# Kernel tuning notes

Hardware: AMD Instinct MI355X
Metric: run time of the kernel (lower is better)

The kernel has to match this reference:

```python
import jax, jax.numpy as jnp
import numpy as np

BOND = 64
RANK = 16
PATCH = 4
SIDE = 64          # num_patches_side = 256 // 4
OUT_C = 3
NODES = [1, 4, 16, 64, 256, 1024]   # per-layer node counts, depth=6
TOTAL_NODES = sum(NODES)            # 1365


def _norm_factor(key, shape):
    f = jax.random.normal(key, shape, dtype=jnp.float32)
    return f / (jnp.linalg.norm(f, axis=-1, keepdims=True) + 1e-8)


def setup_inputs() -> dict:
    key = jax.random.key(0)
    ks = jax.random.split(key, 10)
    B = 128
    x = jax.random.normal(ks[0], (B, 1, BOND), dtype=jnp.float32)
    # All layers' factors concatenated along the node axis (sliced per-layer).
    factor_in = _norm_factor(ks[1], (TOTAL_NODES, RANK, BOND))
    factor_tl = _norm_factor(ks[2], (TOTAL_NODES, RANK, BOND))
    factor_tr = _norm_factor(ks[3], (TOTAL_NODES, RANK, BOND))
    factor_bl = _norm_factor(ks[4], (TOTAL_NODES, RANK, BOND))
    factor_br = _norm_factor(ks[5], (TOTAL_NODES, RANK, BOND))
    scale = 1.0 + 0.02 * jax.random.normal(ks[6], (TOTAL_NODES, RANK), dtype=jnp.float32)
    head_w = jax.random.normal(ks[7], (OUT_C * PATCH * PATCH, BOND), dtype=jnp.float32) * (1.0 / np.sqrt(BOND))
    head_b = jnp.zeros((OUT_C * PATCH * PATCH,), dtype=jnp.float32)
    return {"x": x, "factor_in": factor_in, "factor_tl": factor_tl,
            "factor_tr": factor_tr, "factor_bl": factor_bl, "factor_br": factor_br,
            "scale": scale, "head_w": head_w, "head_b": head_b}


def _forward(x, factor_in, factor_tl, factor_tr, factor_bl, factor_br, scale, head_w, head_b):
    grid = 1
    off = 0
    for n in NODES:  # static loop over depth=6 layers
        fi = factor_in[off:off + n]
        sc = scale[off:off + n]
        lat = jnp.einsum('bni,nri->bnr', x, fi) * sc[None]        # [B,n,r]
        outs = jnp.stack(
            [jnp.einsum('bnr,nro->bno', lat, factor_tl[off:off + n]),
             jnp.einsum('bnr,nro->bno', lat, factor_tr[off:off + n]),
             jnp.einsum('bnr,nro->bno', lat, factor_bl[off:off + n]),
             jnp.einsum('bnr,nro->bno', lat, factor_br[off:off + n])],
            axis=2)                                               # [B,n,4,o]
        x4 = outs + x[:, :, None, :]
        # 'b (h w) (h2 w2) c -> b (h h2 w w2) c' with h=w=grid, h2=w2=2
        b, _, _, c = x4.shape
        x = x4.reshape(b, grid, grid, 2, 2, c).transpose(0, 1, 3, 2, 4, 5).reshape(b, 4 * n, c)
        grid *= 2
        off += n
    # head: Linear(bond -> c*p*p) then 'b (h w) (p1 p2 c) -> b c (h p1) (w p2)'
    y = x @ head_w.T + head_b                                     # [B, 4096, 48]
    b = y.shape[0]
    y = y.reshape(b, SIDE, SIDE, PATCH, PATCH, OUT_C)
    y = y.transpose(0, 5, 1, 3, 2, 4).reshape(b, OUT_C, SIDE * PATCH, SIDE * PATCH)
    return y


def reference(x, factor_in, factor_tl, factor_tr, factor_bl, factor_br, scale, head_w, head_b):
    return _forward(x, factor_in, factor_tl, factor_tr, factor_bl, factor_br, scale, head_w, head_b)
```

## Files before the change

kernel.cpp:

```cpp
#include <hip/hip_runtime.h>

constexpr int BOND = 64;
constexpr int RANK = 16;
constexpr int BT   = 8;
constexpr int NTHR = 256;
constexpr int LPAD = 68;

typedef short  short8 __attribute__((ext_vector_type(8)));
typedef float  f32x4  __attribute__((ext_vector_type(4)));


__device__ __forceinline__ unsigned short f2bf(float f) {
    union { float f; unsigned u; } v; v.f = f;
    unsigned r = v.u + 0x7FFFu + ((v.u >> 16) & 1u);
    return (unsigned short)(r >> 16);
}

__device__ __forceinline__ void node_lat(const float* __restrict__ f_in,
                                         const float* __restrict__ scale,
                                         int fo,
                                         const float* xin,
                                         float* lat,
                                         int tid)
{
    const int b = tid >> 5;
    const int r = (tid >> 1) & 15;
    const int h = tid & 1;
    const float4* fir = (const float4*)(f_in + (size_t)fo * (RANK * BOND) + r * BOND + h * 32);
    const float4* xb  = (const float4*)(xin + b * BOND + h * 32);
    float p = 0.f;
#pragma unroll
    for (int i = 0; i < 8; ++i) {
        const float4 a = fir[i], c = xb[i];
        p += a.x * c.x + a.y * c.y + a.z * c.z + a.w * c.w;
    }
    p += __shfl_xor(p, 1);
    if (h == 0) lat[b * RANK + r] = p * scale[fo * RANK + r];
}

__device__ __forceinline__ void node_children(const float* __restrict__ fd,
                                              const float* xin,
                                              const float* lat,
                                              float* xout,
                                              int bstride,
                                              int tid)
{
    const int o  = tid & 63;
    const int b0 = tid >> 6;
    float f[RANK];
#pragma unroll
    for (int r = 0; r < RANK; ++r) f[r] = fd[r * BOND + o];
#pragma unroll
    for (int bi = 0; bi < BT; bi += 4) {
        const int b = b0 + bi;
        float acc = xin[b * BOND + o];
#pragma unroll
        for (int r = 0; r < RANK; ++r) acc += lat[b * RANK + r] * f[r];
        xout[b * bstride + o] = acc;
    }
}

__global__ __launch_bounds__(NTHR, 3)
void qtree_kernel(const float* __restrict__ x,
                  const float* __restrict__ f_in,
                  const float* __restrict__ f_tl,
                  const float* __restrict__ f_tr,
                  const float* __restrict__ f_bl,
                  const float* __restrict__ f_br,
                  const float* __restrict__ scale,
                  const float* __restrict__ head_w,
                  const float* __restrict__ head_b,
                  float* __restrict__ out)
{
    __shared__ float s_x4[2][BT][BOND];
    __shared__ float s_x5[4][BT][BOND];
    __shared__ float s_leafy[64 * LPAD];
    __shared__ float s_lat[4][BT][RANK];

    const int tid  = threadIdx.x;
    const int lane = tid & 63;
    const int wv   = tid >> 6;
    const int m    = lane & 15;
    const int q    = lane >> 4;
    const int n3   = blockIdx.x;
    const int bg   = blockIdx.y;
    const int jy   = blockIdx.z;
    const int y3   = n3 >> 3, x3 = n3 & 7;

    const float* fdir[4] = { f_tl, f_tr, f_bl, f_br };

    short8 afrag[3][2];
#pragma unroll
    for (int mt = 0; mt < 3; ++mt)
#pragma unroll
        for (int kc = 0; kc < 2; ++kc) {
            const float* src = head_w + (mt * 16 + m) * 64 + kc * 32 + q * 8;
            short8 a;
#pragma unroll
            for (int j = 0; j < 8; ++j) a[j] = (short)f2bf(src[j]);
            afrag[mt][kc] = a;
        }
    f32x4 accinit[3];
#pragma unroll
    for (int mt = 0; mt < 3; ++mt)
#pragma unroll
        for (int r = 0; r < 4; ++r) accinit[mt][r] = head_b[mt * 16 + q * 4 + r];
    const int leaf = wv * 16 + m;
    const int lb = leaf >> 3, ldx = (leaf >> 2) & 1, lc = leaf & 3;
    const int lcy = lc >> 1, lcx = lc & 1;
    const int sy_base = lb * 384 + lcy * 64 + ldx * 8 + lcx * 4;
    int sy_ofs[3][4];
#pragma unroll
    for (int mt = 0; mt < 3; ++mt)
#pragma unroll
        for (int r = 0; r < 4; ++r) {
            const int o = mt * 16 + q * 4 + r;
            sy_ofs[mt][r] = sy_base + (o % 3) * 128 + (o / 12) * 16 + ((o / 3) & 3);
        }

    for (int i4 = tid; i4 < BT * BOND / 4; i4 += NTHR)
        ((float4*)&s_x5[0][0][0])[i4] = ((const float4*)(x + (size_t)bg * BT * BOND))[i4];
    __syncthreads();

    {
        node_lat(f_in, scale, 0, &s_x5[0][0][0], &s_lat[0][0][0], tid);
        __syncthreads();
        const int d = ((y3 >> 2) << 1) | (x3 >> 2);
        node_children(fdir[d], &s_x5[0][0][0], &s_lat[0][0][0], &s_x5[1][0][0], BOND, tid);
        __syncthreads();
    }
    {
        const int fo = 1 + ((y3 >> 2) * 2 + (x3 >> 2));
        node_lat(f_in, scale, fo, &s_x5[1][0][0], &s_lat[0][0][0], tid);
        __syncthreads();
        const int d = (((y3 >> 1) & 1) << 1) | ((x3 >> 1) & 1);
        node_children(fdir[d] + (size_t)fo * RANK * BOND, &s_x5[1][0][0], &s_lat[0][0][0], &s_x5[2][0][0], BOND, tid);
        __syncthreads();
    }
    {
        const int fo = 5 + ((y3 >> 1) * 4 + (x3 >> 1));
        node_lat(f_in, scale, fo, &s_x5[2][0][0], &s_lat[0][0][0], tid);
        __syncthreads();
        const int d = ((y3 & 1) << 1) | (x3 & 1);
        node_children(fdir[d] + (size_t)fo * RANK * BOND, &s_x5[2][0][0], &s_lat[0][0][0], &s_x5[3][0][0], BOND, tid);
        __syncthreads();
    }
    {
        const int fo = 21 + n3;
        node_lat(f_in, scale, fo, &s_x5[3][0][0], &s_lat[0][0][0], tid);
        __syncthreads();
#pragma unroll
        for (int jx = 0; jx < 2; ++jx)
            node_children(fdir[2 * jy + jx] + (size_t)fo * RANK * BOND,
                          &s_x5[3][0][0], &s_lat[0][0][0], &s_x4[jx][0][0], BOND, tid);
        __syncthreads();
    }

    for (int jx = 0; jx < 2; ++jx) {
        const int y4 = 2 * y3 + jy, x4c = 2 * x3 + jx;
        const int fo4 = 85 + y4 * 16 + x4c;
        node_lat(f_in, scale, fo4, &s_x4[jx][0][0], &s_lat[0][0][0], tid);
        __syncthreads();
#pragma unroll
        for (int e = 0; e < 4; ++e)
            node_children(fdir[e] + (size_t)fo4 * RANK * BOND,
                          &s_x4[jx][0][0], &s_lat[0][0][0], &s_x5[e][0][0], BOND, tid);
        __syncthreads();

        int fo5[4];
#pragma unroll
        for (int e = 0; e < 4; ++e) {
            const int dy = e >> 1, dx = e & 1;
            fo5[e] = 341 + (2 * y4 + dy) * 32 + (2 * x4c + dx);
            node_lat(f_in, scale, fo5[e], &s_x5[e][0][0], &s_lat[e][0][0], tid);
        }
        __syncthreads();

        for (int p = 0; p < 2; ++p) {
#pragma unroll
            for (int dx2 = 0; dx2 < 2; ++dx2) {
                const int e = 2 * p + dx2;
#pragma unroll
                for (int c = 0; c < 4; ++c)
                    node_children(fdir[c] + (size_t)fo5[e] * RANK * BOND,
                                  &s_x5[e][0][0], &s_lat[e][0][0],
                                  s_leafy + (dx2 * 4 + c) * LPAD, 8 * LPAD, tid);
            }
            __syncthreads();

            short8 bfrag[2];
#pragma unroll
            for (int kc = 0; kc < 2; ++kc) {
                const float* src = &s_leafy[leaf * LPAD + kc * 32 + q * 8];
                const float4 lo = *(const float4*)src;
                const float4 hi = *(const float4*)(src + 4);
                short8 bq;
                bq[0] = (short)f2bf(lo.x); bq[1] = (short)f2bf(lo.y);
                bq[2] = (short)f2bf(lo.z); bq[3] = (short)f2bf(lo.w);
                bq[4] = (short)f2bf(hi.x); bq[5] = (short)f2bf(hi.y);
                bq[6] = (short)f2bf(hi.z); bq[7] = (short)f2bf(hi.w);
                bfrag[kc] = bq;
            }
            f32x4 acc[3];
#pragma unroll
            for (int mt = 0; mt < 3; ++mt) acc[mt] = accinit[mt];
#pragma unroll
            for (int kc = 0; kc < 2; ++kc)
#pragma unroll
                for (int mt = 0; mt < 3; ++mt)
                    acc[mt] = __builtin_amdgcn_mfma_f32_16x16x32_bf16(afrag[mt][kc], bfrag[kc], acc[mt], 0, 0, 0);
            __syncthreads();

            float* s_y = s_leafy;
#pragma unroll
            for (int mt = 0; mt < 3; ++mt)
#pragma unroll
                for (int r = 0; r < 4; ++r) s_y[sy_ofs[mt][r]] = acc[mt][r];
            __syncthreads();

            const int base_row = (4 * y3 + 2 * jy + p) * 8;
            const int base_col = (4 * x3 + 2 * jx) * 8;
#pragma unroll
            for (int s = 0; s < 3; ++s) {
                const int idx = tid + NTHR * s;
                const int c4  = idx & 3;
                const int r2  = (idx >> 2) & 7;
                const int bc  = idx >> 5;
                const float4 v = *(const float4*)&s_y[(bc * 8 + r2) * 16 + c4 * 4];
                const size_t off = ((size_t)(bg * BT + bc / 3) * 3 + (bc % 3)) * 65536
                                 + (size_t)(base_row + r2) * 256 + base_col + c4 * 4;
                *(float4*)&out[off] = v;
            }
            __syncthreads();
        }
    }
}

extern "C" void kernel_launch(void* const* d_in, const int* in_sizes, int n_in,
                              void* d_out, int out_size, void* d_ws, size_t ws_size,
                              hipStream_t stream) {
    const float* x    = (const float*)d_in[0];
    const float* f_in = (const float*)d_in[1];
    const float* f_tl = (const float*)d_in[2];
    const float* f_tr = (const float*)d_in[3];
    const float* f_bl = (const float*)d_in[4];
    const float* f_br = (const float*)d_in[5];
    const float* sc   = (const float*)d_in[6];
    const float* hw   = (const float*)d_in[7];
    const float* hb   = (const float*)d_in[8];
    float* out = (float*)d_out;

    dim3 grid(64, 16, 2);
    qtree_kernel<<<grid, NTHR, 0, stream>>>(x, f_in, f_tl, f_tr, f_bl, f_br, sc, hw, hb, out);
}
```

Before: 319.6 us.

## Give each wavefront its own two batch rows and drop block-wide barriers

Restructures the tree traversal so each of the four wavefronts owns two batch elements, with private shared-memory buffers for activations, latents, leaf tiles and output staging. All __syncthreads calls go away, since only intra-wave ordering is needed. Leaf activations are stored directly as bf16 in shared memory, so the MFMA B fragment is one vector load instead of a load plus conversion. In exchange, each wave reloads the factor rows for every node (four times the global/L2 factor traffic per block), and the code relies on implicit wave-level ordering of LDS accesses.

```diff
diff --git a/kernel.cpp b/kernel.cpp
--- a/kernel.cpp
+++ b/kernel.cpp
@@ -1,10 +1,6 @@
 #include <hip/hip_runtime.h>
 
-constexpr int BOND = 64;
-constexpr int RANK = 16;
-constexpr int BT   = 8;
 constexpr int NTHR = 256;
-constexpr int LPAD = 68;
 
 typedef short  short8 __attribute__((ext_vector_type(8)));
 typedef float  f32x4  __attribute__((ext_vector_type(4)));
@@ -16,18 +12,18 @@
     return (unsigned short)(r >> 16);
 }
 
-__device__ __forceinline__ void node_lat(const float* __restrict__ f_in,
-                                         const float* __restrict__ scale,
-                                         int fo,
-                                         const float* xin,
-                                         float* lat,
-                                         int tid)
-{
-    const int b = tid >> 5;
-    const int r = (tid >> 1) & 15;
-    const int h = tid & 1;
-    const float4* fir = (const float4*)(f_in + (size_t)fo * (RANK * BOND) + r * BOND + h * 32);
-    const float4* xb  = (const float4*)(xin + b * BOND + h * 32);
+__device__ __forceinline__ void wlat(const float* __restrict__ f_in,
+                                     const float* __restrict__ scale,
+                                     int fo,
+                                     const float (*xin)[64],
+                                     float (*lat)[16],
+                                     int lane)
+{
+    const int b = lane >> 5;
+    const int r = (lane >> 1) & 15;
+    const int h = lane & 1;
+    const float4* fir = (const float4*)(f_in + (size_t)fo * 1024 + r * 64 + h * 32);
+    const float4* xb  = (const float4*)(&xin[b][0] + h * 32);
     float p = 0.f;
 #pragma unroll
     for (int i = 0; i < 8; ++i) {
@@ -35,28 +31,45 @@
         p += a.x * c.x + a.y * c.y + a.z * c.z + a.w * c.w;
     }
     p += __shfl_xor(p, 1);
-    if (h == 0) lat[b * RANK + r] = p * scale[fo * RANK + r];
-}
-
-__device__ __forceinline__ void node_children(const float* __restrict__ fd,
-                                              const float* xin,
-                                              const float* lat,
-                                              float* xout,
-                                              int bstride,
-                                              int tid)
-{
-    const int o  = tid & 63;
-    const int b0 = tid >> 6;
-    float f[RANK];
-#pragma unroll
-    for (int r = 0; r < RANK; ++r) f[r] = fd[r * BOND + o];
-#pragma unroll
-    for (int bi = 0; bi < BT; bi += 4) {
-        const int b = b0 + bi;
-        float acc = xin[b * BOND + o];
-#pragma unroll
-        for (int r = 0; r < RANK; ++r) acc += lat[b * RANK + r] * f[r];
-        xout[b * bstride + o] = acc;
+    if (h == 0) lat[b][r] = p * scale[fo * 16 + r];
+}
+
+__device__ __forceinline__ void wchild(const float* __restrict__ fd,
+                                       const float (*xin)[64],
+                                       const float (*lat)[16],
+                                       float (*xout)[64],
+                                       int lane)
+{
+    const int o = lane;
+    float f[16];
+#pragma unroll
+    for (int r = 0; r < 16; ++r) f[r] = fd[r * 64 + o];
+#pragma unroll
+    for (int b = 0; b < 2; ++b) {
+        float acc = xin[b][o];
+#pragma unroll
+        for (int r = 0; r < 16; ++r) acc += lat[b][r] * f[r];
+        xout[b][o] = acc;
+    }
+}
+
+__device__ __forceinline__ void wchild_leaf(const float* __restrict__ fd,
+                                            const float (*xin)[64],
+                                            const float (*lat)[16],
+                                            unsigned short* leaf,
+                                            int nbase,
+                                            int lane)
+{
+    const int o = lane;
+    float f[16];
+#pragma unroll
+    for (int r = 0; r < 16; ++r) f[r] = fd[r * 64 + o];
+#pragma unroll
+    for (int b = 0; b < 2; ++b) {
+        float acc = xin[b][o];
+#pragma unroll
+        for (int r = 0; r < 16; ++r) acc += lat[b][r] * f[r];
+        leaf[(b * 8 + nbase) * 72 + o] = f2bf(acc);
     }
 }
 
@@ -72,15 +85,18 @@
                   const float* __restrict__ head_b,
                   float* __restrict__ out)
 {
-    __shared__ float s_x4[2][BT][BOND];
-    __shared__ float s_x5[4][BT][BOND];
-    __shared__ float s_leafy[64 * LPAD];
-    __shared__ float s_lat[4][BT][RANK];
+    __shared__ float s_xa[4][2][64];
+    __shared__ float s_xb[4][2][64];
+    __shared__ float s_x4[4][2][2][64];
+    __shared__ float s_x5[4][4][2][64];
+    __shared__ float s_lat[4][2][16];
+    __shared__ unsigned short s_leaf[4][16][72];
+    __shared__ float s_y[4][768];
 
     const int tid  = threadIdx.x;
+    const int wv   = tid >> 6;
     const int lane = tid & 63;
-    const int wv   = tid >> 6;
-    const int m    = lane & 15;
+    const int n    = lane & 15;
     const int q    = lane >> 4;
     const int n3   = blockIdx.x;
     const int bg   = blockIdx.y;
@@ -94,7 +110,7 @@
     for (int mt = 0; mt < 3; ++mt)
 #pragma unroll
         for (int kc = 0; kc < 2; ++kc) {
-            const float* src = head_w + (mt * 16 + m) * 64 + kc * 32 + q * 8;
+            const float* src = head_w + (mt * 16 + n) * 64 + kc * 32 + q * 8;
             short8 a;
 #pragma unroll
             for (int j = 0; j < 8; ++j) a[j] = (short)f2bf(src[j]);
@@ -105,8 +121,7 @@
     for (int mt = 0; mt < 3; ++mt)
 #pragma unroll
         for (int r = 0; r < 4; ++r) accinit[mt][r] = head_b[mt * 16 + q * 4 + r];
-    const int leaf = wv * 16 + m;
-    const int lb = leaf >> 3, ldx = (leaf >> 2) & 1, lc = leaf & 3;
+    const int lb = n >> 3, ldx = (n >> 2) & 1, lc = n & 3;
     const int lcy = lc >> 1, lcx = lc & 1;
     const int sy_base = lb * 384 + lcy * 64 + ldx * 8 + lcx * 4;
     int sy_ofs[3][4];
@@ -118,120 +133,90 @@
             sy_ofs[mt][r] = sy_base + (o % 3) * 128 + (o / 12) * 16 + ((o / 3) & 3);
         }
 
-    for (int i4 = tid; i4 < BT * BOND / 4; i4 += NTHR)
-        ((float4*)&s_x5[0][0][0])[i4] = ((const float4*)(x + (size_t)bg * BT * BOND))[i4];
-    __syncthreads();
-
-    {
-        node_lat(f_in, scale, 0, &s_x5[0][0][0], &s_lat[0][0][0], tid);
-        __syncthreads();
+    float (*xa)[64]  = s_xa[wv];
+    float (*xb)[64]  = s_xb[wv];
+    float (*lat)[16] = s_lat[wv];
+    unsigned short* leaf = &s_leaf[wv][0][0];
+    float* sy = s_y[wv];
+
+#pragma unroll
+    for (int b = 0; b < 2; ++b)
+        xa[b][lane] = x[(size_t)(bg * 8 + wv * 2 + b) * 64 + lane];
+
+    {
+        wlat(f_in, scale, 0, xa, lat, lane);
         const int d = ((y3 >> 2) << 1) | (x3 >> 2);
-        node_children(fdir[d], &s_x5[0][0][0], &s_lat[0][0][0], &s_x5[1][0][0], BOND, tid);
-        __syncthreads();
+        wchild(fdir[d], xa, lat, xb, lane);
     }
     {
         const int fo = 1 + ((y3 >> 2) * 2 + (x3 >> 2));
-        node_lat(f_in, scale, fo, &s_x5[1][0][0], &s_lat[0][0][0], tid);
-        __syncthreads();
+        wlat(f_in, scale, fo, xb, lat, lane);
         const int d = (((y3 >> 1) & 1) << 1) | ((x3 >> 1) & 1);
-        node_children(fdir[d] + (size_t)fo * RANK * BOND, &s_x5[1][0][0], &s_lat[0][0][0], &s_x5[2][0][0], BOND, tid);
-        __syncthreads();
+        wchild(fdir[d] + (size_t)fo * 1024, xb, lat, xa, lane);
     }
     {
         const int fo = 5 + ((y3 >> 1) * 4 + (x3 >> 1));
-        node_lat(f_in, scale, fo, &s_x5[2][0][0], &s_lat[0][0][0], tid);
-        __syncthreads();
+        wlat(f_in, scale, fo, xa, lat, lane);
         const int d = ((y3 & 1) << 1) | (x3 & 1);
-        node_children(fdir[d] + (size_t)fo * RANK * BOND, &s_x5[2][0][0], &s_lat[0][0][0], &s_x5[3][0][0], BOND, tid);
-        __syncthreads();
+        wchild(fdir[d] + (size_t)fo * 1024, xa, lat, xb, lane);
     }
     {
         const int fo = 21 + n3;
-        node_lat(f_in, scale, fo, &s_x5[3][0][0], &s_lat[0][0][0], tid);
-        __syncthreads();
+        wlat(f_in, scale, fo, xb, lat, lane);
 #pragma unroll
         for (int jx = 0; jx < 2; ++jx)
-            node_children(fdir[2 * jy + jx] + (size_t)fo * RANK * BOND,
-                          &s_x5[3][0][0], &s_lat[0][0][0], &s_x4[jx][0][0], BOND, tid);
-        __syncthreads();
+            wchild(fdir[2 * jy + jx] + (size_t)fo * 1024, xb, lat, s_x4[wv][jx], lane);
     }
 
     for (int jx = 0; jx < 2; ++jx) {
         const int y4 = 2 * y3 + jy, x4c = 2 * x3 + jx;
         const int fo4 = 85 + y4 * 16 + x4c;
-        node_lat(f_in, scale, fo4, &s_x4[jx][0][0], &s_lat[0][0][0], tid);
-        __syncthreads();
+        wlat(f_in, scale, fo4, s_x4[wv][jx], lat, lane);
 #pragma unroll
         for (int e = 0; e < 4; ++e)
-            node_children(fdir[e] + (size_t)fo4 * RANK * BOND,
-                          &s_x4[jx][0][0], &s_lat[0][0][0], &s_x5[e][0][0], BOND, tid);
-        __syncthreads();
-
-        int fo5[4];
-#pragma unroll
-        for (int e = 0; e < 4; ++e) {
-            const int dy = e >> 1, dx = e & 1;
-            fo5[e] = 341 + (2 * y4 + dy) * 32 + (2 * x4c + dx);
-            node_lat(f_in, scale, fo5[e], &s_x5[e][0][0], &s_lat[e][0][0], tid);
-        }
-        __syncthreads();
+            wchild(fdir[e] + (size_t)fo4 * 1024, s_x4[wv][jx], lat, s_x5[wv][e], lane);
 
         for (int p = 0; p < 2; ++p) {
 #pragma unroll
             for (int dx2 = 0; dx2 < 2; ++dx2) {
                 const int e = 2 * p + dx2;
+                const int fo5 = 341 + (2 * y4 + p) * 32 + (2 * x4c + dx2);
+                wlat(f_in, scale, fo5, s_x5[wv][e], lat, lane);
 #pragma unroll
                 for (int c = 0; c < 4; ++c)
-                    node_children(fdir[c] + (size_t)fo5[e] * RANK * BOND,
-                                  &s_x5[e][0][0], &s_lat[e][0][0],
-                                  s_leafy + (dx2 * 4 + c) * LPAD, 8 * LPAD, tid);
+                    wchild_leaf(fdir[c] + (size_t)fo5 * 1024, s_x5[wv][e], lat,
+                                leaf, dx2 * 4 + c, lane);
             }
-            __syncthreads();
-
-            short8 bfrag[2];
+
+            f32x4 acc[3];
+#pragma unroll
+            for (int mt = 0; mt < 3; ++mt) acc[mt] = accinit[mt];
 #pragma unroll
             for (int kc = 0; kc < 2; ++kc) {
-                const float* src = &s_leafy[leaf * LPAD + kc * 32 + q * 8];
-                const float4 lo = *(const float4*)src;
-                const float4 hi = *(const float4*)(src + 4);
-                short8 bq;
-                bq[0] = (short)f2bf(lo.x); bq[1] = (short)f2bf(lo.y);
-                bq[2] = (short)f2bf(lo.z); bq[3] = (short)f2bf(lo.w);
-                bq[4] = (short)f2bf(hi.x); bq[5] = (short)f2bf(hi.y);
-                bq[6] = (short)f2bf(hi.z); bq[7] = (short)f2bf(hi.w);
-                bfrag[kc] = bq;
+                const short8 bfrag = *(const short8*)&s_leaf[wv][n][kc * 32 + q * 8];
+#pragma unroll
+                for (int mt = 0; mt < 3; ++mt)
+                    acc[mt] = __builtin_amdgcn_mfma_f32_16x16x32_bf16(afrag[mt][kc], bfrag, acc[mt], 0, 0, 0);
             }
-            f32x4 acc[3];
-#pragma unroll
-            for (int mt = 0; mt < 3; ++mt) acc[mt] = accinit[mt];
-#pragma unroll
-            for (int kc = 0; kc < 2; ++kc)
-#pragma unroll
-                for (int mt = 0; mt < 3; ++mt)
-                    acc[mt] = __builtin_amdgcn_mfma_f32_16x16x32_bf16(afrag[mt][kc], bfrag[kc], acc[mt], 0, 0, 0);
-            __syncthreads();
-
-            float* s_y = s_leafy;
+
 #pragma unroll
             for (int mt = 0; mt < 3; ++mt)
 #pragma unroll
-                for (int r = 0; r < 4; ++r) s_y[sy_ofs[mt][r]] = acc[mt][r];
-            __syncthreads();
+                for (int r = 0; r < 4; ++r) sy[sy_ofs[mt][r]] = acc[mt][r];
 
             const int base_row = (4 * y3 + 2 * jy + p) * 8;
             const int base_col = (4 * x3 + 2 * jx) * 8;
 #pragma unroll
             for (int s = 0; s < 3; ++s) {
-                const int idx = tid + NTHR * s;
-                const int c4  = idx & 3;
-                const int r2  = (idx >> 2) & 7;
-                const int bc  = idx >> 5;
-                const float4 v = *(const float4*)&s_y[(bc * 8 + r2) * 16 + c4 * 4];
-                const size_t off = ((size_t)(bg * BT + bc / 3) * 3 + (bc % 3)) * 65536
+                const int i  = lane + 64 * s;
+                const int c4 = i & 3;
+                const int r2 = (i >> 2) & 7;
+                const int bc = i >> 5;
+                const float4 v = *(const float4*)&sy[(bc * 8 + r2) * 16 + c4 * 4];
+                const size_t off = ((size_t)((bg * 8 + wv * 2 + bc / 3) * 3 + (bc % 3))) * 65536
                                  + (size_t)(base_row + r2) * 256 + base_col + c4 * 4;
                 *(float4*)&out[off] = v;
             }
-            __syncthreads();
         }
     }
 }
```

Result: no change. 317.0 us (-0.8%).
